# Kernel tuning notes

Measured on AMD Instinct MI355X. Metric: run time of the kernel, lower is better.

## Reference

```python
import jax, jax.numpy as jnp
import numpy as np

B, S, HID = 2, 2048, 1024
H, KVH, D = 16, 4, 64
N_REP = H // KVH
SCALE = D ** -0.5
CAP = 50.0


def rotate_half(x):
    x1, x2 = x[..., : D // 2], x[..., D // 2 :]
    return jnp.concatenate((-x2, x1), axis=-1)


def setup_inputs() -> dict:
    key = jax.random.key(0)
    ks = jax.random.split(key, 10)
    X = jax.random.normal(ks[0], (B, S, HID), dtype=jnp.float32)
    # RoPE tables: (B, S, D)
    inv_freq = 1.0 / (10000.0 ** (np.arange(0, D, 2, dtype=np.float32) / D))
    pos = np.arange(S, dtype=np.float32)
    freqs = np.outer(pos, inv_freq)  # (S, D/2)
    emb = np.concatenate([freqs, freqs], axis=-1)  # (S, D)
    cos = jnp.broadcast_to(jnp.asarray(np.cos(emb)), (B, S, D))
    sin = jnp.broadcast_to(jnp.asarray(np.sin(emb)), (B, S, D))
    # causal mask: 1 where key <= query
    mask = jnp.broadcast_to(jnp.tril(jnp.ones((S, S), dtype=jnp.int32)), (B, S, S))
    std = HID ** -0.5
    Wq = jax.random.normal(ks[1], (HID, HID), dtype=jnp.float32) * std
    bq = jnp.zeros((HID,), dtype=jnp.float32)
    Wk = jax.random.normal(ks[2], (KVH * D, HID), dtype=jnp.float32) * std
    bk = jnp.zeros((KVH * D,), dtype=jnp.float32)
    Wv = jax.random.normal(ks[3], (KVH * D, HID), dtype=jnp.float32) * std
    bv = jnp.zeros((KVH * D,), dtype=jnp.float32)
    Wo = jax.random.normal(ks[4], (HID, HID), dtype=jnp.float32) * std
    bo = jnp.zeros((HID,), dtype=jnp.float32)
    return {"X": X, "cos": cos, "sin": sin, "mask": mask,
            "Wq": Wq, "bq": bq, "Wk": Wk, "bk": bk,
            "Wv": Wv, "bv": bv, "Wo": Wo, "bo": bo}


def reference(X, cos, sin, mask, Wq, bq, Wk, bk, Wv, bv, Wo, bo):
    bsz, q_len, _ = X.shape
    q = (X @ Wq.T + bq).reshape(bsz, q_len, H, D).transpose(0, 2, 1, 3)    # (B,H,S,D)
    k = (X @ Wk.T + bk).reshape(bsz, q_len, KVH, D).transpose(0, 2, 1, 3)  # (B,KVH,S,D)
    v = (X @ Wv.T + bv).reshape(bsz, q_len, KVH, D).transpose(0, 2, 1, 3)
    c = cos[:, None, :, :]  # (B,1,S,D)
    s = sin[:, None, :, :]
    q = q * c + rotate_half(q) * s
    k = k * c + rotate_half(k) * s
    k = jnp.repeat(k, N_REP, axis=1)  # GQA expand -> (B,H,S,D)
    v = jnp.repeat(v, N_REP, axis=1)
    scores = jnp.einsum('bhqd,bhkd->bhqk', q, k) * SCALE
    scores = jnp.clip(scores, -CAP, CAP)  # attention cap
    scores = jnp.where(mask[:, None, :, :] == 0, -1e9, scores)
    attn = jax.nn.softmax(scores, axis=-1)  # dropout p=0 -> identity
    ctx = jnp.einsum('bhqk,bhkd->bhqd', attn, v)
    ctx = ctx.transpose(0, 2, 1, 3).reshape(bsz, q_len, H * D)
    out = ctx @ Wo.T + bo
    return (out, attn)
```

## Files before the change

kernel.cpp:

```cpp
#include <hip/hip_runtime.h>
#include <cstdint>
#include <cstddef>

#define S_LEN   2048
#define BATCH   2
#define HID_DIM 1024
#define NHEAD   16
#define NKV     4
#define DHEAD   64
#define SCALE_F 0.125f
#define CAP_F   50.0f

typedef unsigned short u16;
typedef __attribute__((ext_vector_type(8))) short  short8_t;
typedef __attribute__((ext_vector_type(4))) float  f32x4;
typedef __attribute__((ext_vector_type(4))) u16    u16x4;

static __device__ __forceinline__ u16 f2bf(float f) {
  uint32_t x = __builtin_bit_cast(uint32_t, f);
  x += 0x7fffu + ((x >> 16) & 1u);
  return (u16)(x >> 16);
}

static __device__ __forceinline__ void gload_lds16(const void* g, void* l) {
  __builtin_amdgcn_global_load_lds((const __attribute__((address_space(1))) void*)g,
                                   (__attribute__((address_space(3))) void*)l, 16, 0, 0);
}

__global__ void cast_all(const float* __restrict__ X,  u16* __restrict__ xb,
                         const float* __restrict__ Wq, u16* __restrict__ wqb,
                         const float* __restrict__ Wk, u16* __restrict__ wkb,
                         const float* __restrict__ Wv, u16* __restrict__ wvb,
                         const float* __restrict__ Wo, u16* __restrict__ wob) {
  const float* src; u16* dst; int n4;
  switch (blockIdx.y) {
    case 0:  src = X;  dst = xb;  n4 = (BATCH * S_LEN * HID_DIM) / 4; break;
    case 1:  src = Wq; dst = wqb; n4 = (HID_DIM * HID_DIM) / 4;       break;
    case 2:  src = Wk; dst = wkb; n4 = (NKV * DHEAD * HID_DIM) / 4;   break;
    case 3:  src = Wv; dst = wvb; n4 = (NKV * DHEAD * HID_DIM) / 4;   break;
    default: src = Wo; dst = wob; n4 = (HID_DIM * HID_DIM) / 4;       break;
  }
  for (int i = blockIdx.x * 256 + threadIdx.x; i < n4; i += gridDim.x * 256) {
    f32x4 v = ((const f32x4*)src)[i];
    u16x4 o;
    o[0] = f2bf(v[0]); o[1] = f2bf(v[1]); o[2] = f2bf(v[2]); o[3] = f2bf(v[3]);
    ((u16x4*)dst)[i] = o;
  }
}

__global__ __launch_bounds__(256) void gemm_qkv(const u16* __restrict__ Xb,
                                                const u16* __restrict__ Wqb,
                                                const u16* __restrict__ Wkb,
                                                const u16* __restrict__ Wvb,
                                                const float* __restrict__ bq,
                                                const float* __restrict__ bk,
                                                const float* __restrict__ bv,
                                                const float* __restrict__ cosb,
                                                const float* __restrict__ sinb,
                                                u16* __restrict__ qout,
                                                u16* __restrict__ kout,
                                                u16* __restrict__ vtout) {
  __shared__ u16 As[128 * 64];
  __shared__ u16 Bs[128 * 64];
  const int tid = threadIdx.x, lane = tid & 63, wid = tid >> 6;
  const int l15 = lane & 15, lg = lane >> 4;
  const int m0 = blockIdx.x * 128, n0 = blockIdx.y * 128;
  const int wm = wid & 1, wn = wid >> 1;
  const int K = HID_DIM;

  const u16* Wp; const float* biasp; int nl, mode;
  if (n0 < 1024)      { Wp = Wqb; biasp = bq; nl = n0;        mode = 0; }
  else if (n0 < 1280) { Wp = Wkb; biasp = bk; nl = n0 - 1024; mode = 1; }
  else                { Wp = Wvb; biasp = bv; nl = n0 - 1280; mode = 2; }

  f32x4 acc[4][4];
  #pragma unroll
  for (int a = 0; a < 4; ++a)
    #pragma unroll
    for (int b2 = 0; b2 < 4; ++b2) acc[a][b2] = (f32x4){0.f, 0.f, 0.f, 0.f};

  const int srow = (lane >> 3), sg = (lane & 7);

  for (int kk = 0; kk < K; kk += 64) {
    __syncthreads();
    #pragma unroll
    for (int i = 0; i < 4; ++i) {
      const int c = wid * 4 + i;
      const int r = c * 8 + srow;
      const int g = sg ^ (r & 7);
      gload_lds16(Xb + (size_t)(m0 + r) * K + kk + g * 8, As + c * 512);
      gload_lds16(Wp + (size_t)(nl + r) * K + kk + g * 8, Bs + c * 512);
    }
    __syncthreads();
    #pragma unroll
    for (int ks = 0; ks < 2; ++ks) {
      short8_t xa[4], wb[4];
      #pragma unroll
      for (int f = 0; f < 4; ++f) {
        const int rm = wm * 64 + f * 16 + l15;
        const int rn = wn * 64 + f * 16 + l15;
        xa[f] = *(const short8_t*)(As + rm * 64 + (((ks * 4 + lg) ^ (rm & 7)) * 8));
        wb[f] = *(const short8_t*)(Bs + rn * 64 + (((ks * 4 + lg) ^ (rn & 7)) * 8));
      }
      #pragma unroll
      for (int fn = 0; fn < 4; ++fn)
        #pragma unroll
        for (int fm = 0; fm < 4; ++fm)
          acc[fn][fm] = __builtin_amdgcn_mfma_f32_16x16x32_bf16(wb[fn], xa[fm], acc[fn][fm], 0, 0, 0);
    }
  }

  const int m_base = m0 + wm * 64;
  const int nlb = nl + wn * 64;

  if (mode < 2) {
    const int Nout = (mode == 0) ? HID_DIM : (NKV * DHEAD);
    u16* outb = (mode == 0) ? qout : kout;
    #pragma unroll
    for (int fm = 0; fm < 4; ++fm) {
      const int row = m_base + fm * 16 + l15;
      #pragma unroll
      for (int fn = 0; fn < 2; ++fn) {
        const int dh = fn * 16 + lg * 4;
        const f32x4 c4 = *(const f32x4*)(cosb + (size_t)row * 64 + dh);
        const f32x4 s4 = *(const f32x4*)(sinb + (size_t)row * 64 + dh);
        f32x4 x1 = acc[fn][fm]     + *(const f32x4*)(biasp + nlb + fn * 16 + lg * 4);
        f32x4 x2 = acc[fn + 2][fm] + *(const f32x4*)(biasp + nlb + (fn + 2) * 16 + lg * 4);
        f32x4 o1 = x1 * c4 - x2 * s4;
        f32x4 o2 = x2 * c4 + x1 * s4;
        u16x4 u1, u2;
        #pragma unroll
        for (int i = 0; i < 4; ++i) { u1[i] = f2bf(o1[i]); u2[i] = f2bf(o2[i]); }
        *(u16x4*)(outb + (size_t)row * Nout + nlb + fn * 16 + lg * 4)       = u1;
        *(u16x4*)(outb + (size_t)row * Nout + nlb + (fn + 2) * 16 + lg * 4) = u2;
      }
    }
  } else {
    #pragma unroll
    for (int fn = 0; fn < 4; ++fn) {
      const int cb = nlb + fn * 16 + lg * 4;
      #pragma unroll
      for (int fm = 0; fm < 4; ++fm) {
        const int row = m_base + fm * 16 + l15;
        const int b_ = row >> 11, s_ = row & (S_LEN - 1);
        f32x4 v = acc[fn][fm];
        #pragma unroll
        for (int i = 0; i < 4; ++i) {
          vtout[(size_t)(b_ * 256 + cb + i) * S_LEN + s_] = f2bf(v[i] + biasp[cb + i]);
        }
      }
    }
  }
}

__global__ __launch_bounds__(256) void gemm_out(const u16* __restrict__ A,
                                                const u16* __restrict__ W,
                                                const float* __restrict__ bias,
                                                float* __restrict__ outp) {
  __shared__ u16 As[128 * 64];
  __shared__ u16 Bs[128 * 64];
  const int tid = threadIdx.x, lane = tid & 63, wid = tid >> 6;
  const int l15 = lane & 15, lg = lane >> 4;
  const int m0 = blockIdx.x * 128, n0 = blockIdx.y * 128;
  const int wm = wid & 1, wn = wid >> 1;
  const int K = HID_DIM, N = HID_DIM;

  f32x4 acc[4][4];
  #pragma unroll
  for (int a = 0; a < 4; ++a)
    #pragma unroll
    for (int b2 = 0; b2 < 4; ++b2) acc[a][b2] = (f32x4){0.f, 0.f, 0.f, 0.f};

  const int srow = (lane >> 3), sg = (lane & 7);

  for (int kk = 0; kk < K; kk += 64) {
    __syncthreads();
    #pragma unroll
    for (int i = 0; i < 4; ++i) {
      const int c = wid * 4 + i;
      const int r = c * 8 + srow;
      const int g = sg ^ (r & 7);
      gload_lds16(A + (size_t)(m0 + r) * K + kk + g * 8, As + c * 512);
      gload_lds16(W + (size_t)(n0 + r) * K + kk + g * 8, Bs + c * 512);
    }
    __syncthreads();
    #pragma unroll
    for (int ks = 0; ks < 2; ++ks) {
      short8_t xa[4], wb[4];
      #pragma unroll
      for (int f = 0; f < 4; ++f) {
        const int rm = wm * 64 + f * 16 + l15;
        const int rn = wn * 64 + f * 16 + l15;
        xa[f] = *(const short8_t*)(As + rm * 64 + (((ks * 4 + lg) ^ (rm & 7)) * 8));
        wb[f] = *(const short8_t*)(Bs + rn * 64 + (((ks * 4 + lg) ^ (rn & 7)) * 8));
      }
      #pragma unroll
      for (int fn = 0; fn < 4; ++fn)
        #pragma unroll
        for (int fm = 0; fm < 4; ++fm)
          acc[fn][fm] = __builtin_amdgcn_mfma_f32_16x16x32_bf16(wb[fn], xa[fm], acc[fn][fm], 0, 0, 0);
    }
  }

  const int m_base = m0 + wm * 64, n_base = n0 + wn * 64;
  #pragma unroll
  for (int fn = 0; fn < 4; ++fn) {
    const int col = n_base + fn * 16 + lg * 4;
    const f32x4 bvv = *(const f32x4*)(bias + col);
    #pragma unroll
    for (int fm = 0; fm < 4; ++fm) {
      const int row = m_base + fm * 16 + l15;
      *(f32x4*)(outp + (size_t)row * N + col) = acc[fn][fm] + bvv;
    }
  }
}

__global__ __launch_bounds__(256) void attn_fused(const u16* __restrict__ qb,
                                                  const u16* __restrict__ kb,
                                                  const u16* __restrict__ vtb,
                                                  float* __restrict__ attn,
                                                  u16* __restrict__ ctxb) {
  __shared__ u16 kS[2][64 * 64];
  __shared__ u16 vS[2][64 * 64];
  __shared__ u16 pS[4][16][72];

  const int tid = threadIdx.x, lane = tid & 63, wid = tid >> 6;
  const int l15 = lane & 15, lg = lane >> 4;
  const int bh = blockIdx.x, b = bh >> 4, h = bh & 15, kvh = h >> 2;
  const int qt = (int)(gridDim.y - 1 - blockIdx.y);
  const int q0 = qt * 64;
  const int NT = qt + 1;
  const int qw = q0 + wid * 16;
  const int qrow = qw + l15;

  const u16* qp = qb + (size_t)(b * S_LEN + qrow) * HID_DIM + h * DHEAD + lg * 8;
  const short8_t qf0 = *(const short8_t*)qp;
  const short8_t qf1 = *(const short8_t*)(qp + 32);

  const u16* kbase  = kb  + (size_t)(b * S_LEN) * (NKV * DHEAD) + kvh * DHEAD;
  const u16* vtbase = vtb + (size_t)(b * NKV + kvh) * DHEAD * S_LEN;

  const int sr8 = wid * 8 + (lane >> 3);
  const int sg  = lane & 7;

  auto stageK = [&](int bi, int kv0) {
    #pragma unroll
    for (int it = 0; it < 2; ++it) {
      const int r = it * 32 + sr8;
      const int g = sg ^ (r & 7);
      gload_lds16(kbase + (size_t)(kv0 + r) * (NKV * DHEAD) + g * 8,
                  &kS[bi][(it * 32 + wid * 8) * 64]);
    }
  };
  auto stageV = [&](int bi, int kv0) {
    #pragma unroll
    for (int it = 0; it < 2; ++it) {
      const int r = it * 32 + sr8;
      const int g = sg ^ (r & 7);
      gload_lds16(vtbase + (size_t)r * S_LEN + kv0 + g * 8,
                  &vS[bi][(it * 32 + wid * 8) * 64]);
    }
  };

  float lsum = 0.f;
  stageK(0, 0);
  for (int t = 0; t < NT; ++t) {
    const int kv0 = t * 64;
    if (t + 1 < NT) {
      stageK((t + 1) & 1, kv0 + 64);
      asm volatile("s_waitcnt vmcnt(2)" ::: "memory");
    } else {
      asm volatile("s_waitcnt vmcnt(0)" ::: "memory");
    }
    __builtin_amdgcn_s_barrier();
    const u16* ks = kS[t & 1];
    const bool maskc = (t == NT - 1);
    #pragma unroll
    for (int g16 = 0; g16 < 4; ++g16) {
      const int r = g16 * 16 + l15;
      short8_t ka0 = *(const short8_t*)(ks + r * 64 + ((lg ^ (r & 7)) * 8));
      short8_t ka1 = *(const short8_t*)(ks + r * 64 + (((4 + lg) ^ (r & 7)) * 8));
      f32x4 sacc = (f32x4){0.f, 0.f, 0.f, 0.f};
      sacc = __builtin_amdgcn_mfma_f32_16x16x32_bf16(ka0, qf0, sacc, 0, 0, 0);
      sacc = __builtin_amdgcn_mfma_f32_16x16x32_bf16(ka1, qf1, sacc, 0, 0, 0);
      #pragma unroll
      for (int i = 0; i < 4; ++i) {
        float sv = fminf(fmaxf(sacc[i] * SCALE_F, -CAP_F), CAP_F);
        float e = __expf(sv - CAP_F);
        if (maskc) {
          const int kvi = kv0 + g16 * 16 + lg * 4 + i;
          e = (kvi <= qrow) ? e : 0.f;
        }
        lsum += e;
      }
    }
    __builtin_amdgcn_s_barrier();
  }
  lsum += __shfl_xor(lsum, 16);
  lsum += __shfl_xor(lsum, 32);
  const float invl = 1.f / lsum;

  float* abase = attn + (size_t)bh * S_LEN * S_LEN;
  float* arow  = abase + (size_t)qrow * S_LEN;
  f32x4 ctx[4];
  #pragma unroll
  for (int dt = 0; dt < 4; ++dt) ctx[dt] = (f32x4){0.f, 0.f, 0.f, 0.f};

  stageK(0, 0);
  stageV(0, 0);
  for (int t = 0; t < NT; ++t) {
    const int kv0 = t * 64;
    if (t + 1 < NT) {
      stageK((t + 1) & 1, kv0 + 64);
      stageV((t + 1) & 1, kv0 + 64);
      asm volatile("s_waitcnt vmcnt(4)" ::: "memory");
    } else {
      asm volatile("s_waitcnt vmcnt(0)" ::: "memory");
    }
    __builtin_amdgcn_s_barrier();
    const u16* ks = kS[t & 1];
    const u16* vs = vS[t & 1];
    const bool maskc = (t == NT - 1);
    #pragma unroll
    for (int g16 = 0; g16 < 4; ++g16) {
      const int r = g16 * 16 + l15;
      short8_t ka0 = *(const short8_t*)(ks + r * 64 + ((lg ^ (r & 7)) * 8));
      short8_t ka1 = *(const short8_t*)(ks + r * 64 + (((4 + lg) ^ (r & 7)) * 8));
      f32x4 sacc = (f32x4){0.f, 0.f, 0.f, 0.f};
      sacc = __builtin_amdgcn_mfma_f32_16x16x32_bf16(ka0, qf0, sacc, 0, 0, 0);
      sacc = __builtin_amdgcn_mfma_f32_16x16x32_bf16(ka1, qf1, sacc, 0, 0, 0);
      f32x4 pv; u16x4 pb;
      #pragma unroll
      for (int i = 0; i < 4; ++i) {
        float sv = fminf(fmaxf(sacc[i] * SCALE_F, -CAP_F), CAP_F);
        float e = __expf(sv - CAP_F);
        if (maskc) {
          const int kvi = kv0 + g16 * 16 + lg * 4 + i;
          e = (kvi <= qrow) ? e : 0.f;
        }
        float p = e * invl;
        pv[i] = p;
        pb[i] = f2bf(p);
      }
      *(f32x4*)(arow + kv0 + g16 * 16 + lg * 4) = pv;
      *(u16x4*)&pS[wid][l15][g16 * 16 + lg * 4] = pb;
    }
    short8_t pa0 = *(const short8_t*)&pS[wid][l15][lg * 8];
    short8_t pa1 = *(const short8_t*)&pS[wid][l15][32 + lg * 8];
    #pragma unroll
    for (int dt = 0; dt < 4; ++dt) {
      const int r = dt * 16 + l15;
      short8_t bv0 = *(const short8_t*)(vs + r * 64 + ((lg ^ (r & 7)) * 8));
      short8_t bv1 = *(const short8_t*)(vs + r * 64 + (((4 + lg) ^ (r & 7)) * 8));
      ctx[dt] = __builtin_amdgcn_mfma_f32_16x16x32_bf16(pa0, bv0, ctx[dt], 0, 0, 0);
      ctx[dt] = __builtin_amdgcn_mfma_f32_16x16x32_bf16(pa1, bv1, ctx[dt], 0, 0, 0);
    }
    __builtin_amdgcn_s_barrier();
  }

  #pragma unroll
  for (int dt = 0; dt < 4; ++dt)
    #pragma unroll
    for (int i = 0; i < 4; ++i) {
      const int row = qw + lg * 4 + i;
      const int d = dt * 16 + l15;
      ctxb[(size_t)(b * S_LEN + row) * HID_DIM + h * DHEAD + d] = f2bf(ctx[dt][i]);
    }

  const int zc0 = q0 + 64;
  if (zc0 < S_LEN) {
    const f32x4 z = (f32x4){0.f, 0.f, 0.f, 0.f};
    for (int r = wid; r < 64; r += 4) {
      float* rowp = abase + (size_t)(q0 + r) * S_LEN;
      for (int c = zc0 + lane * 4; c < S_LEN; c += 256)
        *(f32x4*)(rowp + c) = z;
    }
  }
}

extern "C" void kernel_launch(void* const* d_in, const int* in_sizes, int n_in,
                              void* d_out, int out_size, void* d_ws, size_t ws_size,
                              hipStream_t stream) {
  (void)in_sizes; (void)n_in; (void)out_size; (void)ws_size;
  const float* X    = (const float*)d_in[0];
  const float* cosb = (const float*)d_in[1];
  const float* sinb = (const float*)d_in[2];
  const float* Wq = (const float*)d_in[4];
  const float* bq = (const float*)d_in[5];
  const float* Wk = (const float*)d_in[6];
  const float* bk = (const float*)d_in[7];
  const float* Wv = (const float*)d_in[8];
  const float* bv = (const float*)d_in[9];
  const float* Wo = (const float*)d_in[10];
  const float* bo = (const float*)d_in[11];

  float* outp  = (float*)d_out;
  float* attnp = outp + (size_t)BATCH * S_LEN * HID_DIM;

  const int M = BATCH * S_LEN;
  u16* ws    = (u16*)d_ws;
  u16* Xb    = ws;
  u16* Wqb   = Xb  + (size_t)M * HID_DIM;
  u16* Wkb   = Wqb + (size_t)HID_DIM * HID_DIM;
  u16* Wvb   = Wkb + (size_t)NKV * DHEAD * HID_DIM;
  u16* Wob   = Wvb + (size_t)NKV * DHEAD * HID_DIM;
  u16* qbuf  = Wob + (size_t)HID_DIM * HID_DIM;
  u16* kbuf  = qbuf + (size_t)M * HID_DIM;
  u16* vtbuf = kbuf + (size_t)M * NKV * DHEAD;
  u16* ctxb  = vtbuf + (size_t)M * NKV * DHEAD;

  cast_all<<<dim3(1024, 5), 256, 0, stream>>>(X, Xb, Wq, Wqb, Wk, Wkb, Wv, Wvb, Wo, Wob);

  gemm_qkv<<<dim3(M / 128, 12), 256, 0, stream>>>(Xb, Wqb, Wkb, Wvb, bq, bk, bv,
                                                  cosb, sinb, qbuf, kbuf, vtbuf);

  attn_fused<<<dim3(BATCH * NHEAD, S_LEN / 64), 256, 0, stream>>>(qbuf, kbuf, vtbuf, attnp, ctxb);

  gemm_out<<<dim3(M / 128, HID_DIM / 128), 256, 0, stream>>>(ctxb, Wob, bo, outp);
}
```

Measured before the change: 223.2 us.

## Widen attention tile to 128 queries with 8 waves and per-wave causal skip

The attention kernel now processes 128 query rows per block using 512 threads, so each staged K/V tile is shared by twice as many waves. Waves whose 16 rows lie entirely above a key tile skip its compute and just write zeros. Exp is computed via fmed3 clamp and exp2. The V-transpose GEMM epilogue and the ctx output swap MFMA operand order so they can emit 4-wide vector stores instead of scalar ones. The risks are lower occupancy from the larger block and idle waves on diagonal tiles.

```diff
diff --git a/kernel.cpp b/kernel.cpp
--- a/kernel.cpp
+++ b/kernel.cpp
@@ -10,6 +10,7 @@
 #define DHEAD   64
 #define SCALE_F 0.125f
 #define CAP_F   50.0f
+#define L2E     1.44269504f
 
 typedef unsigned short u16;
 typedef __attribute__((ext_vector_type(8))) short  short8_t;
@@ -25,6 +26,11 @@
 static __device__ __forceinline__ void gload_lds16(const void* g, void* l) {
   __builtin_amdgcn_global_load_lds((const __attribute__((address_space(1))) void*)g,
                                    (__attribute__((address_space(3))) void*)l, 16, 0, 0);
+}
+
+static __device__ __forceinline__ float expclamp(float x) {
+  float c = __builtin_amdgcn_fmed3f(x, -CAP_F, CAP_F);
+  return __builtin_amdgcn_exp2f(c * L2E - CAP_F * L2E);
 }
 
 __global__ void cast_all(const float* __restrict__ X,  u16* __restrict__ xb,
@@ -102,11 +108,19 @@
         xa[f] = *(const short8_t*)(As + rm * 64 + (((ks * 4 + lg) ^ (rm & 7)) * 8));
         wb[f] = *(const short8_t*)(Bs + rn * 64 + (((ks * 4 + lg) ^ (rn & 7)) * 8));
       }
-      #pragma unroll
-      for (int fn = 0; fn < 4; ++fn)
-        #pragma unroll
-        for (int fm = 0; fm < 4; ++fm)
-          acc[fn][fm] = __builtin_amdgcn_mfma_f32_16x16x32_bf16(wb[fn], xa[fm], acc[fn][fm], 0, 0, 0);
+      if (mode != 2) {
+        #pragma unroll
+        for (int fn = 0; fn < 4; ++fn)
+          #pragma unroll
+          for (int fm = 0; fm < 4; ++fm)
+            acc[fn][fm] = __builtin_amdgcn_mfma_f32_16x16x32_bf16(wb[fn], xa[fm], acc[fn][fm], 0, 0, 0);
+      } else {
+        #pragma unroll
+        for (int fn = 0; fn < 4; ++fn)
+          #pragma unroll
+          for (int fm = 0; fm < 4; ++fm)
+            acc[fn][fm] = __builtin_amdgcn_mfma_f32_16x16x32_bf16(xa[fm], wb[fn], acc[fn][fm], 0, 0, 0);
+      }
     }
   }
 
@@ -138,16 +152,16 @@
   } else {
     #pragma unroll
     for (int fn = 0; fn < 4; ++fn) {
-      const int cb = nlb + fn * 16 + lg * 4;
+      const int d = nlb + fn * 16 + l15;
+      const float bvs = biasp[d];
       #pragma unroll
       for (int fm = 0; fm < 4; ++fm) {
-        const int row = m_base + fm * 16 + l15;
-        const int b_ = row >> 11, s_ = row & (S_LEN - 1);
-        f32x4 v = acc[fn][fm];
-        #pragma unroll
-        for (int i = 0; i < 4; ++i) {
-          vtout[(size_t)(b_ * 256 + cb + i) * S_LEN + s_] = f2bf(v[i] + biasp[cb + i]);
-        }
+        const int s0 = m_base + fm * 16 + lg * 4;
+        const int b_ = s0 >> 11, s_ = s0 & (S_LEN - 1);
+        u16x4 o;
+        #pragma unroll
+        for (int i = 0; i < 4; ++i) o[i] = f2bf(acc[fn][fm][i] + bvs);
+        *(u16x4*)(vtout + (size_t)(b_ * 256 + d) * S_LEN + s_) = o;
       }
     }
   }
@@ -215,21 +229,21 @@
   }
 }
 
-__global__ __launch_bounds__(256) void attn_fused(const u16* __restrict__ qb,
+__global__ __launch_bounds__(512) void attn_fused(const u16* __restrict__ qb,
                                                   const u16* __restrict__ kb,
                                                   const u16* __restrict__ vtb,
                                                   float* __restrict__ attn,
                                                   u16* __restrict__ ctxb) {
   __shared__ u16 kS[2][64 * 64];
   __shared__ u16 vS[2][64 * 64];
-  __shared__ u16 pS[4][16][72];
+  __shared__ u16 pS[8][16][72];
 
   const int tid = threadIdx.x, lane = tid & 63, wid = tid >> 6;
   const int l15 = lane & 15, lg = lane >> 4;
   const int bh = blockIdx.x, b = bh >> 4, h = bh & 15, kvh = h >> 2;
   const int qt = (int)(gridDim.y - 1 - blockIdx.y);
-  const int q0 = qt * 64;
-  const int NT = qt + 1;
+  const int q0 = qt * 128;
+  const int NT = 2 * qt + 2;
   const int qw = q0 + wid * 16;
   const int qrow = qw + l15;
 
@@ -240,26 +254,14 @@
   const u16* kbase  = kb  + (size_t)(b * S_LEN) * (NKV * DHEAD) + kvh * DHEAD;
   const u16* vtbase = vtb + (size_t)(b * NKV + kvh) * DHEAD * S_LEN;
 
-  const int sr8 = wid * 8 + (lane >> 3);
-  const int sg  = lane & 7;
+  const int sr = tid >> 3;
+  const int sg = (tid & 7) ^ (sr & 7);
 
   auto stageK = [&](int bi, int kv0) {
-    #pragma unroll
-    for (int it = 0; it < 2; ++it) {
-      const int r = it * 32 + sr8;
-      const int g = sg ^ (r & 7);
-      gload_lds16(kbase + (size_t)(kv0 + r) * (NKV * DHEAD) + g * 8,
-                  &kS[bi][(it * 32 + wid * 8) * 64]);
-    }
+    gload_lds16(kbase + (size_t)(kv0 + sr) * (NKV * DHEAD) + sg * 8, &kS[bi][tid * 8]);
   };
   auto stageV = [&](int bi, int kv0) {
-    #pragma unroll
-    for (int it = 0; it < 2; ++it) {
-      const int r = it * 32 + sr8;
-      const int g = sg ^ (r & 7);
-      gload_lds16(vtbase + (size_t)r * S_LEN + kv0 + g * 8,
-                  &vS[bi][(it * 32 + wid * 8) * 64]);
-    }
+    gload_lds16(vtbase + (size_t)sr * S_LEN + kv0 + sg * 8, &vS[bi][tid * 8]);
   };
 
   float lsum = 0.f;
@@ -268,30 +270,31 @@
     const int kv0 = t * 64;
     if (t + 1 < NT) {
       stageK((t + 1) & 1, kv0 + 64);
-      asm volatile("s_waitcnt vmcnt(2)" ::: "memory");
+      asm volatile("s_waitcnt vmcnt(1)" ::: "memory");
     } else {
       asm volatile("s_waitcnt vmcnt(0)" ::: "memory");
     }
     __builtin_amdgcn_s_barrier();
-    const u16* ks = kS[t & 1];
-    const bool maskc = (t == NT - 1);
-    #pragma unroll
-    for (int g16 = 0; g16 < 4; ++g16) {
-      const int r = g16 * 16 + l15;
-      short8_t ka0 = *(const short8_t*)(ks + r * 64 + ((lg ^ (r & 7)) * 8));
-      short8_t ka1 = *(const short8_t*)(ks + r * 64 + (((4 + lg) ^ (r & 7)) * 8));
-      f32x4 sacc = (f32x4){0.f, 0.f, 0.f, 0.f};
-      sacc = __builtin_amdgcn_mfma_f32_16x16x32_bf16(ka0, qf0, sacc, 0, 0, 0);
-      sacc = __builtin_amdgcn_mfma_f32_16x16x32_bf16(ka1, qf1, sacc, 0, 0, 0);
-      #pragma unroll
-      for (int i = 0; i < 4; ++i) {
-        float sv = fminf(fmaxf(sacc[i] * SCALE_F, -CAP_F), CAP_F);
-        float e = __expf(sv - CAP_F);
-        if (maskc) {
-          const int kvi = kv0 + g16 * 16 + lg * 4 + i;
-          e = (kvi <= qrow) ? e : 0.f;
+    if (kv0 <= qw + 15) {
+      const u16* ks = kS[t & 1];
+      const bool maskc = (kv0 + 63 > qw);
+      #pragma unroll
+      for (int g16 = 0; g16 < 4; ++g16) {
+        const int r = g16 * 16 + l15;
+        short8_t ka0 = *(const short8_t*)(ks + r * 64 + ((lg ^ (r & 7)) * 8));
+        short8_t ka1 = *(const short8_t*)(ks + r * 64 + (((4 + lg) ^ (r & 7)) * 8));
+        f32x4 sacc = (f32x4){0.f, 0.f, 0.f, 0.f};
+        sacc = __builtin_amdgcn_mfma_f32_16x16x32_bf16(ka0, qf0, sacc, 0, 0, 0);
+        sacc = __builtin_amdgcn_mfma_f32_16x16x32_bf16(ka1, qf1, sacc, 0, 0, 0);
+        #pragma unroll
+        for (int i = 0; i < 4; ++i) {
+          float e = expclamp(sacc[i] * SCALE_F);
+          if (maskc) {
+            const int kvi = kv0 + g16 * 16 + lg * 4 + i;
+            e = (kvi <= qrow) ? e : 0.f;
+          }
+          lsum += e;
         }
-        lsum += e;
       }
     }
     __builtin_amdgcn_s_barrier();
@@ -313,64 +316,69 @@
     if (t + 1 < NT) {
       stageK((t + 1) & 1, kv0 + 64);
       stageV((t + 1) & 1, kv0 + 64);
-      asm volatile("s_waitcnt vmcnt(4)" ::: "memory");
+      asm volatile("s_waitcnt vmcnt(2)" ::: "memory");
     } else {
       asm volatile("s_waitcnt vmcnt(0)" ::: "memory");
     }
     __builtin_amdgcn_s_barrier();
-    const u16* ks = kS[t & 1];
-    const u16* vs = vS[t & 1];
-    const bool maskc = (t == NT - 1);
-    #pragma unroll
-    for (int g16 = 0; g16 < 4; ++g16) {
-      const int r = g16 * 16 + l15;
-      short8_t ka0 = *(const short8_t*)(ks + r * 64 + ((lg ^ (r & 7)) * 8));
-      short8_t ka1 = *(const short8_t*)(ks + r * 64 + (((4 + lg) ^ (r & 7)) * 8));
-      f32x4 sacc = (f32x4){0.f, 0.f, 0.f, 0.f};
-      sacc = __builtin_amdgcn_mfma_f32_16x16x32_bf16(ka0, qf0, sacc, 0, 0, 0);
-      sacc = __builtin_amdgcn_mfma_f32_16x16x32_bf16(ka1, qf1, sacc, 0, 0, 0);
-      f32x4 pv; u16x4 pb;
-      #pragma unroll
-      for (int i = 0; i < 4; ++i) {
-        float sv = fminf(fmaxf(sacc[i] * SCALE_F, -CAP_F), CAP_F);
-        float e = __expf(sv - CAP_F);
-        if (maskc) {
-          const int kvi = kv0 + g16 * 16 + lg * 4 + i;
-          e = (kvi <= qrow) ? e : 0.f;
+    if (kv0 > qw + 15) {
+      const f32x4 z = (f32x4){0.f, 0.f, 0.f, 0.f};
+      #pragma unroll
+      for (int g16 = 0; g16 < 4; ++g16)
+        *(f32x4*)(arow + kv0 + g16 * 16 + lg * 4) = z;
+    } else {
+      const u16* ks = kS[t & 1];
+      const u16* vs = vS[t & 1];
+      const bool maskc = (kv0 + 63 > qw);
+      #pragma unroll
+      for (int g16 = 0; g16 < 4; ++g16) {
+        const int r = g16 * 16 + l15;
+        short8_t ka0 = *(const short8_t*)(ks + r * 64 + ((lg ^ (r & 7)) * 8));
+        short8_t ka1 = *(const short8_t*)(ks + r * 64 + (((4 + lg) ^ (r & 7)) * 8));
+        f32x4 sacc = (f32x4){0.f, 0.f, 0.f, 0.f};
+        sacc = __builtin_amdgcn_mfma_f32_16x16x32_bf16(ka0, qf0, sacc, 0, 0, 0);
+        sacc = __builtin_amdgcn_mfma_f32_16x16x32_bf16(ka1, qf1, sacc, 0, 0, 0);
+        f32x4 pv; u16x4 pb;
+        #pragma unroll
+        for (int i = 0; i < 4; ++i) {
+          float e = expclamp(sacc[i] * SCALE_F);
+          if (maskc) {
+            const int kvi = kv0 + g16 * 16 + lg * 4 + i;
+            e = (kvi <= qrow) ? e : 0.f;
+          }
+          float p = e * invl;
+          pv[i] = p;
+          pb[i] = f2bf(p);
         }
-        float p = e * invl;
-        pv[i] = p;
-        pb[i] = f2bf(p);
-      }
-      *(f32x4*)(arow + kv0 + g16 * 16 + lg * 4) = pv;
-      *(u16x4*)&pS[wid][l15][g16 * 16 + lg * 4] = pb;
-    }
-    short8_t pa0 = *(const short8_t*)&pS[wid][l15][lg * 8];
-    short8_t pa1 = *(const short8_t*)&pS[wid][l15][32 + lg * 8];
-    #pragma unroll
-    for (int dt = 0; dt < 4; ++dt) {
-      const int r = dt * 16 + l15;
-      short8_t bv0 = *(const short8_t*)(vs + r * 64 + ((lg ^ (r & 7)) * 8));
-      short8_t bv1 = *(const short8_t*)(vs + r * 64 + (((4 + lg) ^ (r & 7)) * 8));
-      ctx[dt] = __builtin_amdgcn_mfma_f32_16x16x32_bf16(pa0, bv0, ctx[dt], 0, 0, 0);
-      ctx[dt] = __builtin_amdgcn_mfma_f32_16x16x32_bf16(pa1, bv1, ctx[dt], 0, 0, 0);
+        *(f32x4*)(arow + kv0 + g16 * 16 + lg * 4) = pv;
+        *(u16x4*)&pS[wid][l15][g16 * 16 + lg * 4] = pb;
+      }
+      short8_t pa0 = *(const short8_t*)&pS[wid][l15][lg * 8];
+      short8_t pa1 = *(const short8_t*)&pS[wid][l15][32 + lg * 8];
+      #pragma unroll
+      for (int dt = 0; dt < 4; ++dt) {
+        const int r = dt * 16 + l15;
+        short8_t bv0 = *(const short8_t*)(vs + r * 64 + ((lg ^ (r & 7)) * 8));
+        short8_t bv1 = *(const short8_t*)(vs + r * 64 + (((4 + lg) ^ (r & 7)) * 8));
+        ctx[dt] = __builtin_amdgcn_mfma_f32_16x16x32_bf16(bv0, pa0, ctx[dt], 0, 0, 0);
+        ctx[dt] = __builtin_amdgcn_mfma_f32_16x16x32_bf16(bv1, pa1, ctx[dt], 0, 0, 0);
+      }
     }
     __builtin_amdgcn_s_barrier();
   }
 
   #pragma unroll
-  for (int dt = 0; dt < 4; ++dt)
-    #pragma unroll
-    for (int i = 0; i < 4; ++i) {
-      const int row = qw + lg * 4 + i;
-      const int d = dt * 16 + l15;
-      ctxb[(size_t)(b * S_LEN + row) * HID_DIM + h * DHEAD + d] = f2bf(ctx[dt][i]);
-    }
-
-  const int zc0 = q0 + 64;
+  for (int dt = 0; dt < 4; ++dt) {
+    u16x4 o;
+    #pragma unroll
+    for (int i = 0; i < 4; ++i) o[i] = f2bf(ctx[dt][i]);
+    *(u16x4*)(ctxb + (size_t)(b * S_LEN + qrow) * HID_DIM + h * DHEAD + dt * 16 + lg * 4) = o;
+  }
+
+  const int zc0 = q0 + 128;
   if (zc0 < S_LEN) {
     const f32x4 z = (f32x4){0.f, 0.f, 0.f, 0.f};
-    for (int r = wid; r < 64; r += 4) {
+    for (int r = wid; r < 128; r += 8) {
       float* rowp = abase + (size_t)(q0 + r) * S_LEN;
       for (int c = zc0 + lane * 4; c < S_LEN; c += 256)
         *(f32x4*)(rowp + c) = z;
@@ -414,7 +422,7 @@
   gemm_qkv<<<dim3(M / 128, 12), 256, 0, stream>>>(Xb, Wqb, Wkb, Wvb, bq, bk, bv,
                                                   cosb, sinb, qbuf, kbuf, vtbuf);
 
-  attn_fused<<<dim3(BATCH * NHEAD, S_LEN / 64), 256, 0, stream>>>(qbuf, kbuf, vtbuf, attnp, ctxb);
+  attn_fused<<<dim3(BATCH * NHEAD, S_LEN / 128), 512, 0, stream>>>(qbuf, kbuf, vtbuf, attnp, ctxb);
 
   gemm_out<<<dim3(M / 128, HID_DIM / 128), 256, 0, stream>>>(ctxb, Wob, bo, outp);
 }
```

Result: slower. 229.7 us (+2.9%).
